# Kernel tuning notes

Measured on AMD Instinct MI355X. Metric: run time of the kernel, lower is better.

Reference implementation:

```python
import jax, jax.numpy as jnp
import numpy as np

N = 100000      # nodes
E = 1600000     # edges (avg degree 16)
IN = 128        # input_dim
HID = 32        # hidden_dim per head (layer 1)
HEADS = 2       # heads (layer 1)
OUT = 32        # output_dim (layer 2, heads=1)
NEG_SLOPE = 0.2 # PyG GATConv default leaky relu slope


def setup_inputs() -> dict:
    key = jax.random.key(0)
    ks = jax.random.split(key, 10)
    s = 0.1  # glorot-ish scale
    x = jax.random.normal(ks[0], (N, IN), jnp.float32)
    edge_index = jax.random.randint(ks[1], (2, E), 0, N, dtype=jnp.int64)
    W1 = jax.random.normal(ks[2], (IN, HEADS * HID), jnp.float32) * s
    a1_src = jax.random.normal(ks[3], (HEADS, HID), jnp.float32) * s
    a1_dst = jax.random.normal(ks[4], (HEADS, HID), jnp.float32) * s
    b1 = jnp.zeros((HEADS * HID,), jnp.float32)
    W2 = jax.random.normal(ks[5], (HEADS * HID, OUT), jnp.float32) * s
    a2_src = jax.random.normal(ks[6], (1, OUT), jnp.float32) * s
    a2_dst = jax.random.normal(ks[7], (1, OUT), jnp.float32) * s
    b2 = jnp.zeros((OUT,), jnp.float32)
    return {"x": x, "edge_index": edge_index, "W1": W1, "a1_src": a1_src,
            "a1_dst": a1_dst, "b1": b1, "W2": W2, "a2_src": a2_src,
            "a2_dst": a2_dst, "b2": b2}


def _gat_layer(x, src, dst, W, a_src, a_dst, b, heads, out_ch, concat, n_nodes):
    # linear projection: [N, heads, out_ch]
    h = (x @ W).reshape(n_nodes, heads, out_ch)
    # per-node attention halves: [N, heads]
    alpha_s = jnp.einsum('nhc,hc->nh', h, a_src)
    alpha_d = jnp.einsum('nhc,hc->nh', h, a_dst)
    # per-edge raw score (message x_j = source node, softmax over dst segment)
    e = jax.nn.leaky_relu(alpha_s[src] + alpha_d[dst], NEG_SLOPE)  # [E, heads]
    # segment softmax over incoming edges of each dst node
    m = jax.ops.segment_max(e, dst, num_segments=n_nodes)          # [N, heads]
    m = jax.lax.stop_gradient(m)
    ee = jnp.exp(e - m[dst])
    denom = jax.ops.segment_sum(ee, dst, num_segments=n_nodes)     # [N, heads]
    alpha = ee / (denom[dst] + 1e-16)                              # [E, heads]
    # weighted scatter-add aggregation
    msg = h[src] * alpha[:, :, None]                               # [E, heads, out_ch]
    out = jax.ops.segment_sum(msg, dst, num_segments=n_nodes)      # [N, heads, out_ch]
    if concat:
        out = out.reshape(n_nodes, heads * out_ch)
    else:
        out = out.mean(axis=1)
    return out + b


def reference(x, edge_index, W1, a1_src, a1_dst, b1, W2, a2_src, a2_dst, b2):
    n = x.shape[0]
    # PyG GATConv adds self-loops by default (both layers, same edge set)
    loop = jnp.arange(n, dtype=edge_index.dtype)
    src = jnp.concatenate([edge_index[0], loop])
    dst = jnp.concatenate([edge_index[1], loop])
    h = _gat_layer(x, src, dst, W1, a1_src, a1_dst, b1, HEADS, HID, True, n)
    h = jax.nn.elu(h)
    return _gat_layer(h, src, dst, W2, a2_src, a2_dst, b2, 1, OUT, False, n)
```

## Files before the change

### kernel.cpp

```cpp
#include <hip/hip_runtime.h>
#include <math.h>

#define N_NODES 100000
#define N_EDGES 1600000
#define IN_DIM  128
#define C1      64
#define OUT_DIM 32
#define NEG_SLOPE 0.2f
#define LOG2E 1.44269504f

#define BSHIFT  8
#define BNODES  256
#define NBUCK   ((N_NODES + BNODES - 1) / BNODES)
#define CAP     5120
#define SLOTS   48
#define GC_STRIDE 16
#define G1_BLOCKS ((N_NODES + 127) / 128)
#define B1_BLOCKS ((N_EDGES + 4095) / 4096)

typedef _Float16 half8 __attribute__((ext_vector_type(8)));
typedef float    f32x4 __attribute__((ext_vector_type(4)));

__device__ __forceinline__ float wexp2(float sc) {
    return __builtin_amdgcn_exp2f(fmaxf(sc, NEG_SLOPE * sc));
}

__global__ void prep_k(const float* __restrict__ W1, const float* __restrict__ W2,
                       _Float16* __restrict__ w1t, _Float16* __restrict__ w2t,
                       int* __restrict__ gcur) {
    int t = blockIdx.x * 256 + threadIdx.x;
    if (t < NBUCK * GC_STRIDE) gcur[t] = 0;
    if (t < IN_DIM * C1) {
        int k = t >> 6, n = t & 63;
        w1t[n * IN_DIM + k] = (_Float16)W1[t];
    }
    if (t < C1 * OUT_DIM) {
        int k = t >> 5, n = t & 31;
        w2t[n * C1 + k] = (_Float16)W2[t];
    }
}

__global__ __launch_bounds__(256) void b1g1_k(const int* __restrict__ ei,
        int* __restrict__ gcur, int* __restrict__ buf,
        const float* __restrict__ x, const _Float16* __restrict__ w1t,
        const float* __restrict__ a_s, const float* __restrict__ a_d,
        _Float16* __restrict__ h, float* __restrict__ as_o,
        float* __restrict__ ad_o) {
    __shared__ __align__(16) char smem[29312];
    int t = threadIdx.x;

    if (blockIdx.x < B1_BLOCKS) {
        int*            ledge = (int*)smem;
        unsigned short* lbkt  = (unsigned short*)(smem + 16384);
        int*            scnt  = (int*)(smem + 24576);
        int*            lbase = scnt + NBUCK;
        int*            sbase = lbase + NBUCK;
        for (int i = t; i < NBUCK; i += 256) scnt[i] = 0;
        __syncthreads();
        int pk[16], bk[16], p[16];
        bool v[16];
        #pragma unroll
        for (int i = 0; i < 16; ++i) {
            int e = blockIdx.x * 4096 + i * 256 + t;
            v[i] = e < N_EDGES;
            int ec = v[i] ? e : 0;
            int s = ei[ec];
            int d = ei[N_EDGES + ec];
            bk[i] = d >> BSHIFT;
            pk[i] = s | ((d & (BNODES - 1)) << 17);
            p[i] = v[i] ? atomicAdd(&scnt[bk[i]], 1) : 0;
        }
        __syncthreads();
        int* sA = ledge;
        int* sB = ledge + 512;
        sA[t]       = t < NBUCK ? scnt[t] : 0;
        sA[t + 256] = (t + 256) < NBUCK ? scnt[t + 256] : 0;
        __syncthreads();
        int* pin = sA; int* pout = sB;
        for (int off = 1; off < 512; off <<= 1) {
            pout[t] = pin[t] + (t >= off ? pin[t - off] : 0);
            int k = t + 256;
            pout[k] = pin[k] + (k >= off ? pin[k - off] : 0);
            __syncthreads();
            int* tmp = pin; pin = pout; pout = tmp;
        }
        if (t < NBUCK) {
            lbase[t] = pin[t] - scnt[t];
            sbase[t] = scnt[t] ? atomicAdd(&gcur[t * GC_STRIDE], scnt[t]) : 0;
        }
        {
            int k = t + 256;
            if (k < NBUCK) {
                lbase[k] = pin[k] - scnt[k];
                sbase[k] = scnt[k] ? atomicAdd(&gcur[k * GC_STRIDE], scnt[k]) : 0;
            }
        }
        __syncthreads();
        #pragma unroll
        for (int i = 0; i < 16; ++i) {
            if (v[i]) {
                int slot = lbase[bk[i]] + p[i];
                ledge[slot] = pk[i];
                lbkt[slot] = (unsigned short)bk[i];
            }
        }
        __syncthreads();
        int Eb = N_EDGES - blockIdx.x * 4096;
        if (Eb > 4096) Eb = 4096;
        #pragma unroll
        for (int j = 0; j < 16; ++j) {
            int slot = j * 256 + t;
            if (slot < Eb) {
                int b = lbkt[slot];
                int pos = sbase[b] + (slot - lbase[b]);
                if (pos < CAP) buf[b * CAP + pos] = ledge[slot];
            }
        }
        return;
    }

    _Float16 (*sh)[32 * 72] = (_Float16(*)[32 * 72])smem;
    int wv = t >> 6, lane = t & 63, m = lane & 15, q = lane >> 4;
    int rbw = (blockIdx.x - B1_BLOCKS) * 128 + wv * 32;
    f32x4 acc[2][4];
    #pragma unroll
    for (int i = 0; i < 2; ++i)
        #pragma unroll
        for (int j = 0; j < 4; ++j) acc[i][j] = (f32x4){0.f, 0.f, 0.f, 0.f};
    #pragma unroll
    for (int ks = 0; ks < 4; ++ks) {
        half8 a[2];
        #pragma unroll
        for (int rt = 0; rt < 2; ++rt) {
            int r = rbw + rt * 16 + m;
            r = r < N_NODES ? r : 0;
            const float4* p = (const float4*)(x + (size_t)r * IN_DIM + ks * 32 + q * 8);
            float4 f0 = p[0], f1 = p[1];
            half8 av;
            av[0] = (_Float16)f0.x; av[1] = (_Float16)f0.y;
            av[2] = (_Float16)f0.z; av[3] = (_Float16)f0.w;
            av[4] = (_Float16)f1.x; av[5] = (_Float16)f1.y;
            av[6] = (_Float16)f1.z; av[7] = (_Float16)f1.w;
            a[rt] = av;
        }
        #pragma unroll
        for (int ct = 0; ct < 4; ++ct) {
            half8 b = *(const half8*)(w1t + (ct * 16 + m) * IN_DIM + ks * 32 + q * 8);
            acc[0][ct] = __builtin_amdgcn_mfma_f32_16x16x32_f16(a[0], b, acc[0][ct], 0, 0, 0);
            acc[1][ct] = __builtin_amdgcn_mfma_f32_16x16x32_f16(a[1], b, acc[1][ct], 0, 0, 0);
        }
    }
    _Float16* ws = sh[wv];
    #pragma unroll
    for (int rt = 0; rt < 2; ++rt)
        #pragma unroll
        for (int ct = 0; ct < 4; ++ct)
            #pragma unroll
            for (int r = 0; r < 4; ++r)
                ws[(rt * 16 + q * 4 + r) * 72 + ct * 16 + m] = (_Float16)acc[rt][ct][r];
    __syncthreads();
    int rl = lane >> 1, hp = lane & 1;
    int rg = rbw + rl;
    if (rg < N_NODES) {
        float As_r[32], Ad_r[32];
        const float4* ap = (const float4*)(a_s + hp * 32);
        const float4* dp = (const float4*)(a_d + hp * 32);
        #pragma unroll
        for (int i = 0; i < 8; ++i) {
            float4 v = ap[i];
            As_r[4*i] = v.x; As_r[4*i+1] = v.y; As_r[4*i+2] = v.z; As_r[4*i+3] = v.w;
            float4 u = dp[i];
            Ad_r[4*i] = u.x; Ad_r[4*i+1] = u.y; Ad_r[4*i+2] = u.z; Ad_r[4*i+3] = u.w;
        }
        const _Float16* rowp = ws + rl * 72 + hp * 32;
        half8 c0 = *(const half8*)(rowp);
        half8 c1 = *(const half8*)(rowp + 8);
        half8 c2 = *(const half8*)(rowp + 16);
        half8 c3 = *(const half8*)(rowp + 24);
        float s = 0.f, dd = 0.f;
        #pragma unroll
        for (int j = 0; j < 8; ++j) {
            s  = fmaf((float)c0[j], As_r[j],      s);
            dd = fmaf((float)c0[j], Ad_r[j],      dd);
            s  = fmaf((float)c1[j], As_r[8 + j],  s);
            dd = fmaf((float)c1[j], Ad_r[8 + j],  dd);
            s  = fmaf((float)c2[j], As_r[16 + j], s);
            dd = fmaf((float)c2[j], Ad_r[16 + j], dd);
            s  = fmaf((float)c3[j], As_r[24 + j], s);
            dd = fmaf((float)c3[j], Ad_r[24 + j], dd);
        }
        as_o[rg * 2 + hp] = s  * LOG2E;
        ad_o[rg * 2 + hp] = dd * LOG2E;
        _Float16* hr = h + (size_t)rg * C1 + hp * 32;
        *(half8*)(hr)      = c0;
        *(half8*)(hr + 8)  = c1;
        *(half8*)(hr + 16) = c2;
        *(half8*)(hr + 24) = c3;
    }
}

__global__ __launch_bounds__(256) void binp2_k(const int* __restrict__ gcur,
        const int* __restrict__ buf, int* __restrict__ csr, int* __restrict__ deg) {
    __shared__ int4 lcsr4[BNODES * SLOTS / 4];
    __shared__ int  lcnt[BNODES];
    int* lcsr = (int*)lcsr4;
    int b = blockIdx.x, t = threadIdx.x;
    lcnt[t] = 0;
    __syncthreads();
    int cnt = gcur[b * GC_STRIDE];
    if (cnt > CAP) cnt = CAP;
    const int* bb = buf + b * CAP;
    for (int e = t; e < cnt; e += 256) {
        int vv = bb[e];
        int src = vv & 0x1FFFF;
        int l = vv >> 17;
        int slot = atomicAdd(&lcnt[l], 1);
        if (slot < SLOTS) lcsr[l * SLOTS + slot] = src;
    }
    __syncthreads();
    int c = lcnt[t];
    int slot = c < SLOTS ? c : SLOTS - 1;
    lcsr[t * SLOTS + slot] = b * BNODES + t;
    int cd = c + 1;
    deg[b * BNODES + t] = cd < SLOTS ? cd : SLOTS;
    __syncthreads();
    int4* g4 = (int4*)csr + (size_t)b * (BNODES * SLOTS / 4);
    #pragma unroll
    for (int i = 0; i < BNODES * SLOTS / 4 / 256; ++i)
        g4[t + i * 256] = lcsr4[t + i * 256];
}

__global__ __launch_bounds__(256) void agg1g2_k(const int* __restrict__ deg,
        const int* __restrict__ csr, const _Float16* __restrict__ h1,
        const float* __restrict__ as1, const float* __restrict__ ad1,
        const float* __restrict__ b1, const _Float16* __restrict__ w2t,
        const float* __restrict__ a2s, const float* __restrict__ a2d,
        _Float16* __restrict__ h2, float* __restrict__ as2o,
        float* __restrict__ ad2o) {
    __shared__ int      srow[16 * SLOTS];
    __shared__ _Float16 shu[16 * 72];
    __shared__ _Float16 sh2[16 * 36];
    int t = threadIdx.x;
    int wv = t >> 6, lane = t & 63;
    int dl   = lane >> 4;
    int eg   = (lane >> 3) & 1;
    int cl   = lane & 7;
    int head = cl >> 2;
    int lr   = wv * 4 + dl;
    int d    = blockIdx.x * 16 + lr;

    if (t < 16 * SLOTS / 4)
        ((int4*)srow)[t] = ((const int4*)(csr + (size_t)blockIdx.x * 16 * SLOTS))[t];
    __syncthreads();

    int cnt = deg[d];
    const int* row = srow + lr * SLOTS;
    float advl = ad1[d * 2 + head];
    float acc[8] = {0.f, 0.f, 0.f, 0.f, 0.f, 0.f, 0.f, 0.f};
    float wsum = 0.f;
    for (int base = 0; base < cnt; base += 8) {
        int e0 = base + eg, e1 = e0 + 2, e2 = e0 + 4, e3 = e0 + 6;
        bool v0 = e0 < cnt, v1 = e1 < cnt, v2 = e2 < cnt, v3 = e3 < cnt;
        int s0 = row[v0 ? e0 : 0];
        int s1 = row[v1 ? e1 : 0];
        int s2 = row[v2 ? e2 : 0];
        int s3 = row[v3 ? e3 : 0];
        float a0 = as1[(unsigned)(s0 * 2 + head)];
        float a1 = as1[(unsigned)(s1 * 2 + head)];
        float a2 = as1[(unsigned)(s2 * 2 + head)];
        float a3 = as1[(unsigned)(s3 * 2 + head)];
        half8 g0 = *(const half8*)(h1 + (unsigned)(s0 * C1 + 8 * cl));
        half8 g1 = *(const half8*)(h1 + (unsigned)(s1 * C1 + 8 * cl));
        half8 g2 = *(const half8*)(h1 + (unsigned)(s2 * C1 + 8 * cl));
        half8 g3 = *(const half8*)(h1 + (unsigned)(s3 * C1 + 8 * cl));
        float w0 = v0 ? wexp2(a0 + advl) : 0.f;
        float w1 = v1 ? wexp2(a1 + advl) : 0.f;
        float w2 = v2 ? wexp2(a2 + advl) : 0.f;
        float w3 = v3 ? wexp2(a3 + advl) : 0.f;
        #pragma unroll
        for (int i = 0; i < 8; ++i) {
            acc[i] = fmaf((float)g0[i], w0, acc[i]);
            acc[i] = fmaf((float)g1[i], w1, acc[i]);
            acc[i] = fmaf((float)g2[i], w2, acc[i]);
            acc[i] = fmaf((float)g3[i], w3, acc[i]);
        }
        wsum += (w0 + w1) + (w2 + w3);
    }
    #pragma unroll
    for (int i = 0; i < 8; ++i) acc[i] += __shfl_xor(acc[i], 8);
    wsum += __shfl_xor(wsum, 8);
    if (eg == 0) {
        float inv = 1.f / (wsum + 1e-16f);
        const float4* bv = (const float4*)(b1 + 8 * cl);
        float o[8];
        #pragma unroll
        for (int i = 0; i < 4; ++i) {
            o[i]     = acc[i]     * inv + (&bv[0].x)[i];
            o[4 + i] = acc[4 + i] * inv + (&bv[1].x)[i];
        }
        half8 hv;
        #pragma unroll
        for (int i = 0; i < 8; ++i) {
            float e = o[i] > 0.f ? o[i] : __expf(o[i]) - 1.f;
            hv[i] = (_Float16)e;
        }
        *(half8*)(shu + lr * 72 + cl * 8) = hv;
    }
    __syncthreads();
    if (wv != 0) return;

    {
        int m = lane & 15, q = lane >> 4;
        f32x4 c2[2];
        c2[0] = (f32x4){0.f, 0.f, 0.f, 0.f};
        c2[1] = (f32x4){0.f, 0.f, 0.f, 0.f};
        #pragma unroll
        for (int ks = 0; ks < 2; ++ks) {
            half8 a = *(const half8*)(shu + m * 72 + ks * 32 + q * 8);
            #pragma unroll
            for (int ct = 0; ct < 2; ++ct) {
                half8 b = *(const half8*)(w2t + (ct * 16 + m) * C1 + ks * 32 + q * 8);
                c2[ct] = __builtin_amdgcn_mfma_f32_16x16x32_f16(a, b, c2[ct], 0, 0, 0);
            }
        }
        #pragma unroll
        for (int ct = 0; ct < 2; ++ct)
            #pragma unroll
            for (int r = 0; r < 4; ++r)
                sh2[(q * 4 + r) * 36 + ct * 16 + m] = (_Float16)c2[ct][r];
    }
    asm volatile("s_waitcnt lgkmcnt(0)" ::: "memory");
    __builtin_amdgcn_sched_barrier(0);

    {
        int r = lane & 15, p = lane >> 4;
        int rg = blockIdx.x * 16 + r;
        const float4* ap = (const float4*)(a2s + p * 8);
        const float4* dp = (const float4*)(a2d + p * 8);
        float4 av0 = ap[0], av1 = ap[1];
        float4 dv0 = dp[0], dv1 = dp[1];
        float As[8] = {av0.x, av0.y, av0.z, av0.w, av1.x, av1.y, av1.z, av1.w};
        float Ad[8] = {dv0.x, dv0.y, dv0.z, dv0.w, dv1.x, dv1.y, dv1.z, dv1.w};
        half8 c = *(const half8*)(sh2 + r * 36 + p * 8);
        float s = 0.f, dd = 0.f;
        #pragma unroll
        for (int j = 0; j < 8; ++j) {
            s  = fmaf((float)c[j], As[j], s);
            dd = fmaf((float)c[j], Ad[j], dd);
        }
        s  += __shfl_xor(s, 16);  s  += __shfl_xor(s, 32);
        dd += __shfl_xor(dd, 16); dd += __shfl_xor(dd, 32);
        if (p == 0) {
            as2o[rg] = s  * LOG2E;
            ad2o[rg] = dd * LOG2E;
        }
        *(half8*)(h2 + (size_t)rg * OUT_DIM + p * 8) = c;
    }
}

__global__ __launch_bounds__(256) void agg2_k(const int* __restrict__ deg,
        const int* __restrict__ csr, const _Float16* __restrict__ h2,
        const float* __restrict__ as2, const float* __restrict__ ad2,
        const float* __restrict__ b2, float* __restrict__ out) {
    __shared__ int srow[32 * SLOTS];
    int t = threadIdx.x;
    int wv = t >> 6, lane = t & 63;
    int dl   = lane >> 3;
    int eg   = (lane >> 2) & 1;
    int cl   = lane & 3;
    int lr   = wv * 8 + dl;
    int d    = blockIdx.x * 32 + lr;

    {
        int4* s4 = (int4*)srow;
        const int4* g4 = (const int4*)(csr + (size_t)blockIdx.x * 32 * SLOTS);
        s4[t] = g4[t];
        if (t < 128) s4[256 + t] = g4[256 + t];
    }
    __syncthreads();

    int cnt = deg[d];
    const int* row = srow + lr * SLOTS;
    float advl = ad2[d];
    float acc[8] = {0.f, 0.f, 0.f, 0.f, 0.f, 0.f, 0.f, 0.f};
    float wsum = 0.f;
    for (int base = 0; base < cnt; base += 8) {
        int e0 = base + eg, e1 = e0 + 2, e2 = e0 + 4, e3 = e0 + 6;
        bool v0 = e0 < cnt, v1 = e1 < cnt, v2 = e2 < cnt, v3 = e3 < cnt;
        int s0 = row[v0 ? e0 : 0];
        int s1 = row[v1 ? e1 : 0];
        int s2 = row[v2 ? e2 : 0];
        int s3 = row[v3 ? e3 : 0];
        float a0 = as2[(unsigned)s0];
        float a1 = as2[(unsigned)s1];
        float a2 = as2[(unsigned)s2];
        float a3 = as2[(unsigned)s3];
        half8 g0 = *(const half8*)(h2 + (unsigned)(s0 * OUT_DIM + 8 * cl));
        half8 g1 = *(const half8*)(h2 + (unsigned)(s1 * OUT_DIM + 8 * cl));
        half8 g2 = *(const half8*)(h2 + (unsigned)(s2 * OUT_DIM + 8 * cl));
        half8 g3 = *(const half8*)(h2 + (unsigned)(s3 * OUT_DIM + 8 * cl));
        float w0 = v0 ? wexp2(a0 + advl) : 0.f;
        float w1 = v1 ? wexp2(a1 + advl) : 0.f;
        float w2 = v2 ? wexp2(a2 + advl) : 0.f;
        float w3 = v3 ? wexp2(a3 + advl) : 0.f;
        #pragma unroll
        for (int i = 0; i < 8; ++i) {
            acc[i] = fmaf((float)g0[i], w0, acc[i]);
            acc[i] = fmaf((float)g1[i], w1, acc[i]);
            acc[i] = fmaf((float)g2[i], w2, acc[i]);
            acc[i] = fmaf((float)g3[i], w3, acc[i]);
        }
        wsum += (w0 + w1) + (w2 + w3);
    }
    #pragma unroll
    for (int i = 0; i < 8; ++i) acc[i] += __shfl_xor(acc[i], 4);
    wsum += __shfl_xor(wsum, 4);
    if (eg == 0) {
        float inv = 1.f / (wsum + 1e-16f);
        const float4* bv = (const float4*)(b2 + 8 * cl);
        float4 o0, o1;
        o0.x = acc[0] * inv + bv[0].x; o0.y = acc[1] * inv + bv[0].y;
        o0.z = acc[2] * inv + bv[0].z; o0.w = acc[3] * inv + bv[0].w;
        o1.x = acc[4] * inv + bv[1].x; o1.y = acc[5] * inv + bv[1].y;
        o1.z = acc[6] * inv + bv[1].z; o1.w = acc[7] * inv + bv[1].w;
        float4* ow = (float4*)(out + (size_t)d * OUT_DIM + 8 * cl);
        ow[0] = o0;
        ow[1] = o1;
    }
}


extern "C" void kernel_launch(void* const* d_in, const int* in_sizes, int n_in,
                              void* d_out, int out_size, void* d_ws, size_t ws_size,
                              hipStream_t stream) {
    const float* x   = (const float*)d_in[0];
    const int*   ei  = (const int*)d_in[1];
    const float* W1  = (const float*)d_in[2];
    const float* a1s = (const float*)d_in[3];
    const float* a1d = (const float*)d_in[4];
    const float* b1  = (const float*)d_in[5];
    const float* W2  = (const float*)d_in[6];
    const float* a2s = (const float*)d_in[7];
    const float* a2d = (const float*)d_in[8];
    const float* b2  = (const float*)d_in[9];
    float* out = (float*)d_out;

    char* ws = (char*)d_ws;
    size_t off = 0;
    auto alloc = [&](size_t bytes) -> void* {
        void* p = ws + off;
        off = (off + bytes + 255) & ~(size_t)255;
        return p;
    };
    int* gcur      = (int*)alloc((size_t)NBUCK * GC_STRIDE * 4);
    int* buf       = (int*)alloc((size_t)NBUCK * CAP * 4);
    int* csr       = (int*)alloc((size_t)NBUCK * BNODES * SLOTS * 4);
    int* deg       = (int*)alloc((size_t)NBUCK * BNODES * 4);
    _Float16* w1t  = (_Float16*)alloc((size_t)IN_DIM * C1 * 2);
    _Float16* w2t  = (_Float16*)alloc((size_t)C1 * OUT_DIM * 2);
    _Float16* h1   = (_Float16*)alloc((size_t)N_NODES * C1 * 2);
    float* as1     = (float*)alloc((size_t)N_NODES * 2 * 4);
    float* ad1     = (float*)alloc((size_t)N_NODES * 2 * 4);
    _Float16* h2   = (_Float16*)alloc((size_t)N_NODES * OUT_DIM * 2);
    float* as2     = (float*)alloc((size_t)N_NODES * 4);
    float* ad2     = (float*)alloc((size_t)N_NODES * 4);

    prep_k<<<(IN_DIM * C1 + 255) / 256, 256, 0, stream>>>(W1, W2, w1t, w2t, gcur);
    b1g1_k<<<B1_BLOCKS + G1_BLOCKS, 256, 0, stream>>>(ei, gcur, buf,
                                                      x, w1t, a1s, a1d, h1, as1, ad1);
    binp2_k<<<NBUCK, 256, 0, stream>>>(gcur, buf, csr, deg);
    agg1g2_k<<<N_NODES / 16, 256, 0, stream>>>(deg, csr, h1, as1, ad1, b1,
                                               w2t, a2s, a2d, h2, as2, ad2);
    agg2_k<<<N_NODES / 32, 256, 0, stream>>>(deg, csr, h2, as2, ad2, b2, out);
}
```

Before: 201.3 us.

## Sort nodes by degree within buckets to balance aggregation warps

The binning kernel now builds a per-bucket counting sort of destination nodes by degree and writes a permutation array. Both aggregation kernels process nodes in permuted order, so nodes of similar degree share a wavefront, which reduces divergence from the uneven per-node edge loops. In exchange, CSR rows are gathered indirectly through the permutation, and padding nodes beyond N up to the bucket boundary are now processed, so the buffers are enlarged to the padded size. Writes to the output are guarded for the padded nodes.

```diff
diff --git a/kernel.cpp b/kernel.cpp
--- a/kernel.cpp
+++ b/kernel.cpp
@@ -12,6 +12,7 @@
 #define BSHIFT  8
 #define BNODES  256
 #define NBUCK   ((N_NODES + BNODES - 1) / BNODES)
+#define NPAD    (NBUCK * BNODES)
 #define CAP     5120
 #define SLOTS   48
 #define GC_STRIDE 16
@@ -200,12 +201,15 @@
 }
 
 __global__ __launch_bounds__(256) void binp2_k(const int* __restrict__ gcur,
-        const int* __restrict__ buf, int* __restrict__ csr, int* __restrict__ deg) {
+        const int* __restrict__ buf, int* __restrict__ csr, int* __restrict__ deg,
+        int* __restrict__ perm) {
     __shared__ int4 lcsr4[BNODES * SLOTS / 4];
     __shared__ int  lcnt[BNODES];
+    __shared__ int  dh[SLOTS + 1], dbase[SLOTS + 1];
     int* lcsr = (int*)lcsr4;
     int b = blockIdx.x, t = threadIdx.x;
     lcnt[t] = 0;
+    if (t <= SLOTS) dh[t] = 0;
     __syncthreads();
     int cnt = gcur[b * GC_STRIDE];
     if (cnt > CAP) cnt = CAP;
@@ -222,7 +226,16 @@
     int slot = c < SLOTS ? c : SLOTS - 1;
     lcsr[t * SLOTS + slot] = b * BNODES + t;
     int cd = c + 1;
-    deg[b * BNODES + t] = cd < SLOTS ? cd : SLOTS;
+    if (cd > SLOTS) cd = SLOTS;
+    deg[b * BNODES + t] = cd;
+    int r = atomicAdd(&dh[cd], 1);
+    __syncthreads();
+    if (t == 0) {
+        int s = 0;
+        for (int i = 0; i <= SLOTS; ++i) { dbase[i] = s; s += dh[i]; }
+    }
+    __syncthreads();
+    perm[b * BNODES + dbase[cd] + r] = b * BNODES + t;
     __syncthreads();
     int4* g4 = (int4*)csr + (size_t)b * (BNODES * SLOTS / 4);
     #pragma unroll
@@ -230,13 +243,15 @@
         g4[t + i * 256] = lcsr4[t + i * 256];
 }
 
-__global__ __launch_bounds__(256) void agg1g2_k(const int* __restrict__ deg,
+__global__ __launch_bounds__(256) void agg1g2_k(const int* __restrict__ perm,
+        const int* __restrict__ deg,
         const int* __restrict__ csr, const _Float16* __restrict__ h1,
         const float* __restrict__ as1, const float* __restrict__ ad1,
         const float* __restrict__ b1, const _Float16* __restrict__ w2t,
         const float* __restrict__ a2s, const float* __restrict__ a2d,
         _Float16* __restrict__ h2, float* __restrict__ as2o,
         float* __restrict__ ad2o) {
+    __shared__ int      sperm[16];
     __shared__ int      srow[16 * SLOTS];
     __shared__ _Float16 shu[16 * 72];
     __shared__ _Float16 sh2[16 * 36];
@@ -247,11 +262,16 @@
     int cl   = lane & 7;
     int head = cl >> 2;
     int lr   = wv * 4 + dl;
-    int d    = blockIdx.x * 16 + lr;
-
-    if (t < 16 * SLOTS / 4)
-        ((int4*)srow)[t] = ((const int4*)(csr + (size_t)blockIdx.x * 16 * SLOTS))[t];
-    __syncthreads();
+
+    if (t < 16) sperm[t] = perm[blockIdx.x * 16 + t];
+    __syncthreads();
+    if (t < 192) {
+        int pd = sperm[t / 12];
+        ((int4*)srow)[t] = ((const int4*)csr)[(size_t)pd * 12 + (t % 12)];
+    }
+    __syncthreads();
+
+    int d = sperm[lr];
 
     int cnt = deg[d];
     const int* row = srow + lr * SLOTS;
@@ -334,7 +354,7 @@
 
     {
         int r = lane & 15, p = lane >> 4;
-        int rg = blockIdx.x * 16 + r;
+        int rg = sperm[r];
         const float4* ap = (const float4*)(a2s + p * 8);
         const float4* dp = (const float4*)(a2d + p * 8);
         float4 av0 = ap[0], av1 = ap[1];
@@ -358,10 +378,12 @@
     }
 }
 
-__global__ __launch_bounds__(256) void agg2_k(const int* __restrict__ deg,
+__global__ __launch_bounds__(256) void agg2_k(const int* __restrict__ perm,
+        const int* __restrict__ deg,
         const int* __restrict__ csr, const _Float16* __restrict__ h2,
         const float* __restrict__ as2, const float* __restrict__ ad2,
         const float* __restrict__ b2, float* __restrict__ out) {
+    __shared__ int sperm[32];
     __shared__ int srow[32 * SLOTS];
     int t = threadIdx.x;
     int wv = t >> 6, lane = t & 63;
@@ -369,16 +391,23 @@
     int eg   = (lane >> 2) & 1;
     int cl   = lane & 3;
     int lr   = wv * 8 + dl;
-    int d    = blockIdx.x * 32 + lr;
-
+
+    if (t < 32) sperm[t] = perm[blockIdx.x * 32 + t];
+    __syncthreads();
     {
         int4* s4 = (int4*)srow;
-        const int4* g4 = (const int4*)(csr + (size_t)blockIdx.x * 32 * SLOTS);
-        s4[t] = g4[t];
-        if (t < 128) s4[256 + t] = g4[256 + t];
-    }
-    __syncthreads();
-
+        const int4* c4 = (const int4*)csr;
+        int pd = sperm[t / 12];
+        s4[t] = c4[(size_t)pd * 12 + (t % 12)];
+        int i2 = t + 256;
+        if (i2 < 384) {
+            int pd2 = sperm[i2 / 12];
+            s4[i2] = c4[(size_t)pd2 * 12 + (i2 % 12)];
+        }
+    }
+    __syncthreads();
+
+    int d = sperm[lr];
     int cnt = deg[d];
     const int* row = srow + lr * SLOTS;
     float advl = ad2[d];
@@ -415,7 +444,7 @@
     #pragma unroll
     for (int i = 0; i < 8; ++i) acc[i] += __shfl_xor(acc[i], 4);
     wsum += __shfl_xor(wsum, 4);
-    if (eg == 0) {
+    if (eg == 0 && d < N_NODES) {
         float inv = 1.f / (wsum + 1e-16f);
         const float4* bv = (const float4*)(b2 + 8 * cl);
         float4 o0, o1;
@@ -454,22 +483,23 @@
     };
     int* gcur      = (int*)alloc((size_t)NBUCK * GC_STRIDE * 4);
     int* buf       = (int*)alloc((size_t)NBUCK * CAP * 4);
-    int* csr       = (int*)alloc((size_t)NBUCK * BNODES * SLOTS * 4);
-    int* deg       = (int*)alloc((size_t)NBUCK * BNODES * 4);
+    int* csr       = (int*)alloc((size_t)NPAD * SLOTS * 4);
+    int* deg       = (int*)alloc((size_t)NPAD * 4);
+    int* perm      = (int*)alloc((size_t)NPAD * 4);
     _Float16* w1t  = (_Float16*)alloc((size_t)IN_DIM * C1 * 2);
     _Float16* w2t  = (_Float16*)alloc((size_t)C1 * OUT_DIM * 2);
-    _Float16* h1   = (_Float16*)alloc((size_t)N_NODES * C1 * 2);
-    float* as1     = (float*)alloc((size_t)N_NODES * 2 * 4);
-    float* ad1     = (float*)alloc((size_t)N_NODES * 2 * 4);
-    _Float16* h2   = (_Float16*)alloc((size_t)N_NODES * OUT_DIM * 2);
-    float* as2     = (float*)alloc((size_t)N_NODES * 4);
-    float* ad2     = (float*)alloc((size_t)N_NODES * 4);
+    _Float16* h1   = (_Float16*)alloc((size_t)NPAD * C1 * 2);
+    float* as1     = (float*)alloc((size_t)NPAD * 2 * 4);
+    float* ad1     = (float*)alloc((size_t)NPAD * 2 * 4);
+    _Float16* h2   = (_Float16*)alloc((size_t)NPAD * OUT_DIM * 2);
+    float* as2     = (float*)alloc((size_t)NPAD * 4);
+    float* ad2     = (float*)alloc((size_t)NPAD * 4);
 
     prep_k<<<(IN_DIM * C1 + 255) / 256, 256, 0, stream>>>(W1, W2, w1t, w2t, gcur);
     b1g1_k<<<B1_BLOCKS + G1_BLOCKS, 256, 0, stream>>>(ei, gcur, buf,
                                                       x, w1t, a1s, a1d, h1, as1, ad1);
-    binp2_k<<<NBUCK, 256, 0, stream>>>(gcur, buf, csr, deg);
-    agg1g2_k<<<N_NODES / 16, 256, 0, stream>>>(deg, csr, h1, as1, ad1, b1,
-                                               w2t, a2s, a2d, h2, as2, ad2);
-    agg2_k<<<N_NODES / 32, 256, 0, stream>>>(deg, csr, h2, as2, ad2, b2, out);
-}
+    binp2_k<<<NBUCK, 256, 0, stream>>>(gcur, buf, csr, deg, perm);
+    agg1g2_k<<<NPAD / 16, 256, 0, stream>>>(perm, deg, csr, h1, as1, ad1, b1,
+                                            w2t, a2s, a2d, h2, as2, ad2);
+    agg2_k<<<NPAD / 32, 256, 0, stream>>>(perm, deg, csr, h2, as2, ad2, b2, out);
+}
```

New measurement: 214.6 us. 1.07x slower.
